# Kernel optimization log

Hardware: AMD Instinct MI355X
Metric: run time of the kernel (lower is better)

The kernel has to match this reference:

```python
import jax, jax.numpy as jnp
import numpy as np

D_IN, D_HID, N_TOK = 2048, 8192, 8192

def _ternary(key, shape):
    # ternary {-1, 0, 1} weights stored as float32
    return jax.random.randint(key, shape, -1, 2).astype(jnp.float32)

def setup_inputs() -> dict:
    key = jax.random.key(0)
    kx, k1, k2, kh, k3 = jax.random.split(key, 5)
    return {
        "x": jax.random.normal(kx, (N_TOK, D_IN), dtype=jnp.float32),
        "W1": _ternary(k1, (D_HID, D_IN)),   # gate proj
        "W2": _ternary(k2, (D_HID, D_IN)),   # value proj
        "Wh": _ternary(kh, (D_HID, D_HID)),  # hidden layer (depth-1 == 1)
        "W3": _ternary(k3, (D_IN, D_HID)),   # output proj
        # per-layer dequant scales (scalar), ~1/sqrt(fan_in)
        "s1": jnp.float32(1.0 / np.sqrt(D_IN)),
        "s2": jnp.float32(1.0 / np.sqrt(D_IN)),
        "sh": jnp.float32(1.0 / np.sqrt(D_HID)),
        "s3": jnp.float32(1.0 / np.sqrt(D_HID)),
    }

def _tlin(x, W, s):
    # ternary packed linear: dequantized matmul, no bias
    return jnp.einsum('td,hd->th', x, W) * s

def reference(x, W1, W2, Wh, W3, s1, s2, sh, s3):
    h = jax.nn.silu(_tlin(x, W1, s1)) * _tlin(x, W2, s2)   # SwiGLU entry
    h = jax.nn.gelu(_tlin(h, Wh, sh), approximate=False)    # hidden block (depth-1)
    return _tlin(h, W3, s3)                                 # [N_TOK, D_IN]
```

## Files before the change

### kernel.cpp

```cpp
#include <hip/hip_runtime.h>
#include <hip/hip_bf16.h>
#include <stdint.h>

typedef __bf16 bf16;
typedef __bf16 bf16x8 __attribute__((ext_vector_type(8)));
typedef float f32x4 __attribute__((ext_vector_type(4)));

typedef uint32_t __attribute__((address_space(1))) * gptr_as1;
typedef uint32_t __attribute__((address_space(3))) * lptr_as3;

__device__ __forceinline__ void async16(const void* g, void* l) {
    __builtin_amdgcn_global_load_lds((gptr_as1)(uintptr_t)g,
                                     (lptr_as3)(uintptr_t)l,
                                     16, 0, 0);
}

__device__ __forceinline__ void bar() {
    asm volatile("" ::: "memory");
    __builtin_amdgcn_s_barrier();
    asm volatile("" ::: "memory");
}

__global__ void cvt_f32_bf16_kernel(const float* __restrict__ src,
                                    bf16* __restrict__ dst, int n8) {
    int i = blockIdx.x * blockDim.x + threadIdx.x;
    if (i >= n8) return;
    const float4* s = reinterpret_cast<const float4*>(src);
    float4 a = s[2 * (size_t)i], b = s[2 * (size_t)i + 1];
    bf16x8 v;
    v[0] = (bf16)a.x; v[1] = (bf16)a.y; v[2] = (bf16)a.z; v[3] = (bf16)a.w;
    v[4] = (bf16)b.x; v[5] = (bf16)b.y; v[6] = (bf16)b.z; v[7] = (bf16)b.w;
    *reinterpret_cast<bf16x8*>(dst + (size_t)i * 8) = v;
}

__global__ __launch_bounds__(256, 2)
void gemm12_swiglu(const bf16* __restrict__ A, const bf16* __restrict__ B1,
                   const bf16* __restrict__ B2, bf16* __restrict__ H,
                   const float* __restrict__ s1p, const float* __restrict__ s2p,
                   int N, int K) {
    __shared__ __align__(16) bf16 As[128][64];
    __shared__ __align__(16) bf16 B1s[128][64];
    __shared__ __align__(16) bf16 B2s[128][64];

    const int tid = threadIdx.x;
    const int w = tid >> 6, l = tid & 63;
    const int bn = blockIdx.x, bm = blockIdx.y;
    const int wr = w >> 1, wc = w & 1;

    f32x4 acc1[4][4] = {};
    f32x4 acc2[4][4] = {};

    const int srow = w * 8 + (l >> 3);
    const int scol = (l & 7) * 8;
    const bf16* Ab  = A  + (size_t)(bm * 128 + srow) * K + scol;
    const bf16* B1b = B1 + (size_t)(bn * 128 + srow) * K + scol;
    const bf16* B2b = B2 + (size_t)(bn * 128 + srow) * K + scol;
    char* AsB  = (char*)&As[0][0]  + w * 1024;
    char* B1sB = (char*)&B1s[0][0] + w * 1024;
    char* B2sB = (char*)&B2s[0][0] + w * 1024;

    for (int k0 = 0; k0 < K; k0 += 64) {
#pragma unroll
        for (int r = 0; r < 4; ++r) {
            async16(Ab  + (size_t)r * 32 * K + k0, AsB  + r * 4096);
            async16(B1b + (size_t)r * 32 * K + k0, B1sB + r * 4096);
            async16(B2b + (size_t)r * 32 * K + k0, B2sB + r * 4096);
        }
        __syncthreads();
#pragma unroll
        for (int kk = 0; kk < 64; kk += 32) {
            const int kc = kk + (l >> 4) * 8;
            const int rr = l & 15;
            bf16x8 av[4], b1v[4], b2v[4];
#pragma unroll
            for (int i = 0; i < 4; ++i)
                av[i] = *reinterpret_cast<const bf16x8*>(&As[wr * 64 + i * 16 + rr][kc]);
#pragma unroll
            for (int j = 0; j < 4; ++j)
                b1v[j] = *reinterpret_cast<const bf16x8*>(&B1s[wc * 64 + j * 16 + rr][kc]);
#pragma unroll
            for (int j = 0; j < 4; ++j)
                b2v[j] = *reinterpret_cast<const bf16x8*>(&B2s[wc * 64 + j * 16 + rr][kc]);
#pragma unroll
            for (int i = 0; i < 4; ++i)
#pragma unroll
                for (int j = 0; j < 4; ++j) {
                    acc1[i][j] = __builtin_amdgcn_mfma_f32_16x16x32_bf16(av[i], b1v[j], acc1[i][j], 0, 0, 0);
                    acc2[i][j] = __builtin_amdgcn_mfma_f32_16x16x32_bf16(av[i], b2v[j], acc2[i][j], 0, 0, 0);
                }
        }
        __syncthreads();
    }

    const float s1 = s1p[0], s2 = s2p[0];
    const int row0 = bm * 128 + wr * 64 + (l >> 4) * 4;
    const int col0 = bn * 128 + wc * 64 + (l & 15);
#pragma unroll
    for (int i = 0; i < 4; ++i)
#pragma unroll
        for (int j = 0; j < 4; ++j)
#pragma unroll
            for (int q = 0; q < 4; ++q) {
                float g = acc1[i][j][q] * s1;
                float v = acc2[i][j][q] * s2;
                float sig = 1.0f / (1.0f + __expf(-g));
                H[(size_t)(row0 + i * 16 + q) * N + (col0 + j * 16)] = (bf16)(g * sig * v);
            }
}

template <int EPI>
__global__ __launch_bounds__(512, 1)
void gemm8p(const bf16* __restrict__ A, const bf16* __restrict__ B,
            void* __restrict__ Cout, const float* __restrict__ sp,
            int N, int K) {
    __shared__ __align__(16) char sm[131072];

    const int tid = threadIdx.x;
    const int w = tid >> 6, l = tid & 63;
    const int wr = w >> 2, wc = w & 3;

    const int gx = gridDim.x;
    const int nwg = gx * (int)gridDim.y;
    const int orig = blockIdx.y * gx + blockIdx.x;
    const int wg = (orig & 7) * (nwg >> 3) + (orig >> 3);
    const int bm = wg / gx, bn = wg % gx;

    const int NT = K >> 6;

    f32x4 acc[8][4] = {};

    char* const bufA0 = sm;
    char* const bufB0 = sm + 32768;
    char* const bufA1 = sm + 65536;
    char* const bufB1 = sm + 98304;
    const int arow = bm * 256, brow = bn * 256;

    const int srow_in = l >> 3;
    const int scolb = ((l & 7) ^ srow_in) << 4;
    auto STAGE = [&](char* ldsT, const bf16* g, int grow0, int kt, int r0) {
        const int rr = r0 + w * 8 + srow_in;
        const char* gp = (const char*)(g + (size_t)(grow0 + rr) * K + kt * 64) + scolb;
        async16(gp, ldsT + r0 * 128 + w * 1024);
    };

    const int rlane = l & 15;
    const int chi = (l >> 4) << 4;
    auto FRAG = [&](const char* tb, int row, int ks) -> bf16x8 {
        const int cb = (ks * 64 + chi) ^ ((row & 7) << 4);
        return *reinterpret_cast<const bf16x8*>(tb + row * 128 + cb);
    };

    STAGE(bufB0, B, brow, 0, 0);   STAGE(bufB0, B, brow, 0, 64);
    STAGE(bufB0, B, brow, 0, 128); STAGE(bufB0, B, brow, 0, 192);
    STAGE(bufA0, A, arow, 0, 0);   STAGE(bufA0, A, arow, 0, 128);
    STAGE(bufA0, A, arow, 0, 64);  STAGE(bufA0, A, arow, 0, 192);
    STAGE(bufB1, B, brow, 1, 0);   STAGE(bufB1, B, brow, 1, 64);
    STAGE(bufB1, B, brow, 1, 128); STAGE(bufB1, B, brow, 1, 192);
    STAGE(bufA1, A, arow, 1, 0);   STAGE(bufA1, A, arow, 1, 128);
    asm volatile("s_waitcnt vmcnt(6)" ::: "memory");
    bar();

    for (int kt = 0; kt < NT; ++kt) {
        char* cA = (kt & 1) ? bufA1 : bufA0;
        char* cB = (kt & 1) ? bufB1 : bufB0;
        char* nA = (kt & 1) ? bufA0 : bufA1;

        bf16x8 av[8], bv[8];
#pragma unroll
        for (int j = 0; j < 4; ++j)
#pragma unroll
            for (int ks = 0; ks < 2; ++ks)
                bv[j * 2 + ks] = FRAG(cB, wc * 64 + j * 16 + rlane, ks);
#pragma unroll
        for (int i = 0; i < 4; ++i)
#pragma unroll
            for (int ks = 0; ks < 2; ++ks)
                av[i * 2 + ks] = FRAG(cA, wr * 128 + i * 16 + rlane, ks);
        if (kt + 1 < NT) { STAGE(nA, A, arow, kt + 1, 64); STAGE(nA, A, arow, kt + 1, 192); }
        bar();
        asm volatile("s_waitcnt lgkmcnt(0)" ::: "memory");
        __builtin_amdgcn_sched_barrier(0);
        __builtin_amdgcn_s_setprio(1);
#pragma unroll
        for (int i = 0; i < 4; ++i)
#pragma unroll
            for (int j = 0; j < 2; ++j)
#pragma unroll
                for (int ks = 0; ks < 2; ++ks)
                    acc[i][j] = __builtin_amdgcn_mfma_f32_16x16x32_bf16(av[i * 2 + ks], bv[j * 2 + ks], acc[i][j], 0, 0, 0);
        __builtin_amdgcn_s_setprio(0);
        bar();
        if (kt + 2 < NT) { STAGE(cB, B, brow, kt + 2, 0); STAGE(cB, B, brow, kt + 2, 64); }
        bar();
        __builtin_amdgcn_s_setprio(1);
#pragma unroll
        for (int i = 0; i < 4; ++i)
#pragma unroll
            for (int j = 2; j < 4; ++j)
#pragma unroll
                for (int ks = 0; ks < 2; ++ks)
                    acc[i][j] = __builtin_amdgcn_mfma_f32_16x16x32_bf16(av[i * 2 + ks], bv[j * 2 + ks], acc[i][j], 0, 0, 0);
        __builtin_amdgcn_s_setprio(0);
        bar();
        bf16x8 ah[8];
#pragma unroll
        for (int i = 0; i < 4; ++i)
#pragma unroll
            for (int ks = 0; ks < 2; ++ks)
                ah[i * 2 + ks] = FRAG(cA, wr * 128 + 64 + i * 16 + rlane, ks);
        if (kt + 2 < NT) { STAGE(cB, B, brow, kt + 2, 128); STAGE(cB, B, brow, kt + 2, 192); }
        bar();
        asm volatile("s_waitcnt lgkmcnt(0)" ::: "memory");
        __builtin_amdgcn_sched_barrier(0);
        __builtin_amdgcn_s_setprio(1);
#pragma unroll
        for (int i = 0; i < 4; ++i)
#pragma unroll
            for (int j = 0; j < 2; ++j)
#pragma unroll
                for (int ks = 0; ks < 2; ++ks)
                    acc[4 + i][j] = __builtin_amdgcn_mfma_f32_16x16x32_bf16(ah[i * 2 + ks], bv[j * 2 + ks], acc[4 + i][j], 0, 0, 0);
        __builtin_amdgcn_s_setprio(0);
        bar();
        if (kt + 2 < NT) { STAGE(cA, A, arow, kt + 2, 0); STAGE(cA, A, arow, kt + 2, 128); }
        bar();
        __builtin_amdgcn_s_setprio(1);
#pragma unroll
        for (int i = 0; i < 4; ++i)
#pragma unroll
            for (int j = 2; j < 4; ++j)
#pragma unroll
                for (int ks = 0; ks < 2; ++ks)
                    acc[4 + i][j] = __builtin_amdgcn_mfma_f32_16x16x32_bf16(ah[i * 2 + ks], bv[j * 2 + ks], acc[4 + i][j], 0, 0, 0);
        __builtin_amdgcn_s_setprio(0);
        if (kt == NT - 2) { asm volatile("s_waitcnt vmcnt(0)" ::: "memory"); }
        else              { asm volatile("s_waitcnt vmcnt(6)" ::: "memory"); }
        bar();
    }

    const float s = sp[0];
    const int r0 = bm * 256 + wr * 128 + ((l >> 4) << 2);
    const int c0 = bn * 256 + wc * 64 + rlane;
#pragma unroll
    for (int i = 0; i < 8; ++i)
#pragma unroll
        for (int j = 0; j < 4; ++j)
#pragma unroll
            for (int q = 0; q < 4; ++q) {
                float v = acc[i][j][q] * s;
                size_t idx = (size_t)(r0 + i * 16 + q) * N + (c0 + j * 16);
                if constexpr (EPI == 0) {
                    float g = 0.5f * v * (1.0f + erff(v * 0.70710678118654752f));
                    ((bf16*)Cout)[idx] = (bf16)g;
                } else {
                    ((float*)Cout)[idx] = v;
                }
            }
}

extern "C" void kernel_launch(void* const* d_in, const int* in_sizes, int n_in,
                              void* d_out, int out_size, void* d_ws, size_t ws_size,
                              hipStream_t stream) {
    constexpr int NTOK = 8192, DIN = 2048, DHID = 8192;

    const float* x  = (const float*)d_in[0];
    const float* W1 = (const float*)d_in[1];
    const float* W2 = (const float*)d_in[2];
    const float* Wh = (const float*)d_in[3];
    const float* W3 = (const float*)d_in[4];
    const float* s1 = (const float*)d_in[5];
    const float* s2 = (const float*)d_in[6];
    const float* sh = (const float*)d_in[7];
    const float* s3 = (const float*)d_in[8];
    float* out = (float*)d_out;

    char* ws = (char*)d_ws;
    size_t off = 0;
    bf16* xb  = (bf16*)(ws + off); off += (size_t)NTOK * DIN * 2;
    bf16* w1b = (bf16*)(ws + off); off += (size_t)DHID * DIN * 2;
    bf16* w2b = (bf16*)(ws + off); off += (size_t)DHID * DIN * 2;
    bf16* w3b = (bf16*)(ws + off); off += (size_t)DIN * DHID * 2;
    bf16* whb = (bf16*)(ws + off); off += (size_t)DHID * DHID * 2;
    bf16* h1  = (bf16*)(ws + off); off += (size_t)NTOK * DHID * 2;
    bf16* h2  = (bf16*)(ws + off); off += (size_t)NTOK * DHID * 2;
    if (ws_size < off) return;

    auto cvt = [&](const float* s, bf16* d, size_t n) {
        int n8 = (int)(n / 8);
        cvt_f32_bf16_kernel<<<(n8 + 255) / 256, 256, 0, stream>>>(s, d, n8);
    };
    cvt(x,  xb,  (size_t)NTOK * DIN);
    cvt(W1, w1b, (size_t)DHID * DIN);
    cvt(W2, w2b, (size_t)DHID * DIN);
    cvt(W3, w3b, (size_t)DIN * DHID);
    cvt(Wh, whb, (size_t)DHID * DHID);

    gemm12_swiglu<<<dim3(DHID / 128, NTOK / 128), 256, 0, stream>>>(
        xb, w1b, w2b, h1, s1, s2, DHID, DIN);
    gemm8p<0><<<dim3(DHID / 256, NTOK / 256), 512, 0, stream>>>(
        h1, whb, h2, sh, DHID, DHID);
    gemm8p<1><<<dim3(DIN / 256, NTOK / 256), 512, 0, stream>>>(
        h2, w3b, out, s3, DIN, DHID);
}
```

Before: 1.886 ms.

## Fuse gate/value GEMM into pipelined kernel via interleaved W1/W2 layout

Drops the simple 128x128 SwiGLU GEMM kernel. W1 and W2 are now converted into one interleaved weight buffer, alternating 16-row blocks of gate and value rows, so the optimized 256x256 double-buffered gemm8p kernel can run the first layer with a SwiGLU epilogue that pairs adjacent accumulator tiles. The main loop is also reordered into quadrant-wise fragment loads with explicit buffer swapping, and K becomes a template constant. The aim is to replace the slower first-layer kernel with the better-pipelined one, at the cost of a more intricate staging and wait schedule.

```diff
diff --git a/kernel.cpp b/kernel.cpp
--- a/kernel.cpp
+++ b/kernel.cpp
@@ -33,86 +33,26 @@
     *reinterpret_cast<bf16x8*>(dst + (size_t)i * 8) = v;
 }
 
-__global__ __launch_bounds__(256, 2)
-void gemm12_swiglu(const bf16* __restrict__ A, const bf16* __restrict__ B1,
-                   const bf16* __restrict__ B2, bf16* __restrict__ H,
-                   const float* __restrict__ s1p, const float* __restrict__ s2p,
-                   int N, int K) {
-    __shared__ __align__(16) bf16 As[128][64];
-    __shared__ __align__(16) bf16 B1s[128][64];
-    __shared__ __align__(16) bf16 B2s[128][64];
-
-    const int tid = threadIdx.x;
-    const int w = tid >> 6, l = tid & 63;
-    const int bn = blockIdx.x, bm = blockIdx.y;
-    const int wr = w >> 1, wc = w & 1;
-
-    f32x4 acc1[4][4] = {};
-    f32x4 acc2[4][4] = {};
-
-    const int srow = w * 8 + (l >> 3);
-    const int scol = (l & 7) * 8;
-    const bf16* Ab  = A  + (size_t)(bm * 128 + srow) * K + scol;
-    const bf16* B1b = B1 + (size_t)(bn * 128 + srow) * K + scol;
-    const bf16* B2b = B2 + (size_t)(bn * 128 + srow) * K + scol;
-    char* AsB  = (char*)&As[0][0]  + w * 1024;
-    char* B1sB = (char*)&B1s[0][0] + w * 1024;
-    char* B2sB = (char*)&B2s[0][0] + w * 1024;
-
-    for (int k0 = 0; k0 < K; k0 += 64) {
-#pragma unroll
-        for (int r = 0; r < 4; ++r) {
-            async16(Ab  + (size_t)r * 32 * K + k0, AsB  + r * 4096);
-            async16(B1b + (size_t)r * 32 * K + k0, B1sB + r * 4096);
-            async16(B2b + (size_t)r * 32 * K + k0, B2sB + r * 4096);
-        }
-        __syncthreads();
-#pragma unroll
-        for (int kk = 0; kk < 64; kk += 32) {
-            const int kc = kk + (l >> 4) * 8;
-            const int rr = l & 15;
-            bf16x8 av[4], b1v[4], b2v[4];
-#pragma unroll
-            for (int i = 0; i < 4; ++i)
-                av[i] = *reinterpret_cast<const bf16x8*>(&As[wr * 64 + i * 16 + rr][kc]);
-#pragma unroll
-            for (int j = 0; j < 4; ++j)
-                b1v[j] = *reinterpret_cast<const bf16x8*>(&B1s[wc * 64 + j * 16 + rr][kc]);
-#pragma unroll
-            for (int j = 0; j < 4; ++j)
-                b2v[j] = *reinterpret_cast<const bf16x8*>(&B2s[wc * 64 + j * 16 + rr][kc]);
-#pragma unroll
-            for (int i = 0; i < 4; ++i)
-#pragma unroll
-                for (int j = 0; j < 4; ++j) {
-                    acc1[i][j] = __builtin_amdgcn_mfma_f32_16x16x32_bf16(av[i], b1v[j], acc1[i][j], 0, 0, 0);
-                    acc2[i][j] = __builtin_amdgcn_mfma_f32_16x16x32_bf16(av[i], b2v[j], acc2[i][j], 0, 0, 0);
-                }
-        }
-        __syncthreads();
-    }
-
-    const float s1 = s1p[0], s2 = s2p[0];
-    const int row0 = bm * 128 + wr * 64 + (l >> 4) * 4;
-    const int col0 = bn * 128 + wc * 64 + (l & 15);
-#pragma unroll
-    for (int i = 0; i < 4; ++i)
-#pragma unroll
-        for (int j = 0; j < 4; ++j)
-#pragma unroll
-            for (int q = 0; q < 4; ++q) {
-                float g = acc1[i][j][q] * s1;
-                float v = acc2[i][j][q] * s2;
-                float sig = 1.0f / (1.0f + __expf(-g));
-                H[(size_t)(row0 + i * 16 + q) * N + (col0 + j * 16)] = (bf16)(g * sig * v);
-            }
-}
-
-template <int EPI>
+__global__ void cvt_ilv_kernel(const float* __restrict__ src,
+                               bf16* __restrict__ dst, int n8, int sel) {
+    int i = blockIdx.x * blockDim.x + threadIdx.x;
+    if (i >= n8) return;
+    const int row = i >> 8;
+    const int c = i & 255;
+    const int drow = ((row >> 4) << 5) + (sel << 4) + (row & 15);
+    const float4* s = reinterpret_cast<const float4*>(src);
+    float4 a = s[2 * (size_t)i], b = s[2 * (size_t)i + 1];
+    bf16x8 v;
+    v[0] = (bf16)a.x; v[1] = (bf16)a.y; v[2] = (bf16)a.z; v[3] = (bf16)a.w;
+    v[4] = (bf16)b.x; v[5] = (bf16)b.y; v[6] = (bf16)b.z; v[7] = (bf16)b.w;
+    *reinterpret_cast<bf16x8*>(dst + ((size_t)drow * 256 + c) * 8) = v;
+}
+
+template <int EPI, int K>
 __global__ __launch_bounds__(512, 1)
 void gemm8p(const bf16* __restrict__ A, const bf16* __restrict__ B,
-            void* __restrict__ Cout, const float* __restrict__ sp,
-            int N, int K) {
+            void* __restrict__ Cout, const float* __restrict__ s1p,
+            const float* __restrict__ s2p, int N, int ldh) {
     __shared__ __align__(16) char sm[131072];
 
     const int tid = threadIdx.x;
@@ -125,7 +65,7 @@
     const int wg = (orig & 7) * (nwg >> 3) + (orig >> 3);
     const int bm = wg / gx, bn = wg % gx;
 
-    const int NT = K >> 6;
+    constexpr int NT = K / 64;
 
     f32x4 acc[8][4] = {};
 
@@ -154,29 +94,30 @@
     STAGE(bufB0, B, brow, 0, 128); STAGE(bufB0, B, brow, 0, 192);
     STAGE(bufA0, A, arow, 0, 0);   STAGE(bufA0, A, arow, 0, 128);
     STAGE(bufA0, A, arow, 0, 64);  STAGE(bufA0, A, arow, 0, 192);
+    STAGE(bufA1, A, arow, 1, 0);   STAGE(bufA1, A, arow, 1, 128);
     STAGE(bufB1, B, brow, 1, 0);   STAGE(bufB1, B, brow, 1, 64);
     STAGE(bufB1, B, brow, 1, 128); STAGE(bufB1, B, brow, 1, 192);
-    STAGE(bufA1, A, arow, 1, 0);   STAGE(bufA1, A, arow, 1, 128);
     asm volatile("s_waitcnt vmcnt(6)" ::: "memory");
     bar();
 
+    char* cA = bufA0; char* cB = bufB0;
+    char* nA = bufA1; char* nB = bufB1;
+
+#pragma unroll 1
     for (int kt = 0; kt < NT; ++kt) {
-        char* cA = (kt & 1) ? bufA1 : bufA0;
-        char* cB = (kt & 1) ? bufB1 : bufB0;
-        char* nA = (kt & 1) ? bufA0 : bufA1;
-
-        bf16x8 av[8], bv[8];
-#pragma unroll
-        for (int j = 0; j < 4; ++j)
-#pragma unroll
-            for (int ks = 0; ks < 2; ++ks)
-                bv[j * 2 + ks] = FRAG(cB, wc * 64 + j * 16 + rlane, ks);
-#pragma unroll
-        for (int i = 0; i < 4; ++i)
-#pragma unroll
-            for (int ks = 0; ks < 2; ++ks)
-                av[i * 2 + ks] = FRAG(cA, wr * 128 + i * 16 + rlane, ks);
+        bf16x8 avl[8], bvl[4], bvh[4], avh[8];
+#pragma unroll
+        for (int i = 0; i < 4; ++i)
+#pragma unroll
+            for (int ks = 0; ks < 2; ++ks)
+                avl[i * 2 + ks] = FRAG(cA, wr * 128 + i * 16 + rlane, ks);
+#pragma unroll
+        for (int j = 0; j < 2; ++j)
+#pragma unroll
+            for (int ks = 0; ks < 2; ++ks)
+                bvl[j * 2 + ks] = FRAG(cB, wc * 64 + j * 16 + rlane, ks);
         if (kt + 1 < NT) { STAGE(nA, A, arow, kt + 1, 64); STAGE(nA, A, arow, kt + 1, 192); }
+        asm volatile("s_waitcnt lgkmcnt(8)" ::: "memory");
         bar();
         asm volatile("s_waitcnt lgkmcnt(0)" ::: "memory");
         __builtin_amdgcn_sched_barrier(0);
@@ -187,28 +128,15 @@
             for (int j = 0; j < 2; ++j)
 #pragma unroll
                 for (int ks = 0; ks < 2; ++ks)
-                    acc[i][j] = __builtin_amdgcn_mfma_f32_16x16x32_bf16(av[i * 2 + ks], bv[j * 2 + ks], acc[i][j], 0, 0, 0);
-        __builtin_amdgcn_s_setprio(0);
-        bar();
-        if (kt + 2 < NT) { STAGE(cB, B, brow, kt + 2, 0); STAGE(cB, B, brow, kt + 2, 64); }
-        bar();
-        __builtin_amdgcn_s_setprio(1);
-#pragma unroll
-        for (int i = 0; i < 4; ++i)
-#pragma unroll
-            for (int j = 2; j < 4; ++j)
-#pragma unroll
-                for (int ks = 0; ks < 2; ++ks)
-                    acc[i][j] = __builtin_amdgcn_mfma_f32_16x16x32_bf16(av[i * 2 + ks], bv[j * 2 + ks], acc[i][j], 0, 0, 0);
-        __builtin_amdgcn_s_setprio(0);
-        bar();
-        bf16x8 ah[8];
-#pragma unroll
-        for (int i = 0; i < 4; ++i)
-#pragma unroll
-            for (int ks = 0; ks < 2; ++ks)
-                ah[i * 2 + ks] = FRAG(cA, wr * 128 + 64 + i * 16 + rlane, ks);
-        if (kt + 2 < NT) { STAGE(cB, B, brow, kt + 2, 128); STAGE(cB, B, brow, kt + 2, 192); }
+                    acc[i][j] = __builtin_amdgcn_mfma_f32_16x16x32_bf16(avl[i * 2 + ks], bvl[j * 2 + ks], acc[i][j], 0, 0, 0);
+        __builtin_amdgcn_s_setprio(0);
+        bar();
+#pragma unroll
+        for (int j = 0; j < 2; ++j)
+#pragma unroll
+            for (int ks = 0; ks < 2; ++ks)
+                bvh[j * 2 + ks] = FRAG(cB, wc * 64 + 32 + j * 16 + rlane, ks);
+        if (kt + 2 < NT) { STAGE(cA, A, arow, kt + 2, 0); STAGE(cA, A, arow, kt + 2, 128); }
         bar();
         asm volatile("s_waitcnt lgkmcnt(0)" ::: "memory");
         __builtin_amdgcn_sched_barrier(0);
@@ -219,43 +147,81 @@
             for (int j = 0; j < 2; ++j)
 #pragma unroll
                 for (int ks = 0; ks < 2; ++ks)
-                    acc[4 + i][j] = __builtin_amdgcn_mfma_f32_16x16x32_bf16(ah[i * 2 + ks], bv[j * 2 + ks], acc[4 + i][j], 0, 0, 0);
-        __builtin_amdgcn_s_setprio(0);
-        bar();
-        if (kt + 2 < NT) { STAGE(cA, A, arow, kt + 2, 0); STAGE(cA, A, arow, kt + 2, 128); }
-        bar();
-        __builtin_amdgcn_s_setprio(1);
-#pragma unroll
-        for (int i = 0; i < 4; ++i)
-#pragma unroll
-            for (int j = 2; j < 4; ++j)
-#pragma unroll
-                for (int ks = 0; ks < 2; ++ks)
-                    acc[4 + i][j] = __builtin_amdgcn_mfma_f32_16x16x32_bf16(ah[i * 2 + ks], bv[j * 2 + ks], acc[4 + i][j], 0, 0, 0);
+                    acc[i][2 + j] = __builtin_amdgcn_mfma_f32_16x16x32_bf16(avl[i * 2 + ks], bvh[j * 2 + ks], acc[i][2 + j], 0, 0, 0);
+        __builtin_amdgcn_s_setprio(0);
+        bar();
+#pragma unroll
+        for (int i = 0; i < 4; ++i)
+#pragma unroll
+            for (int ks = 0; ks < 2; ++ks)
+                avh[i * 2 + ks] = FRAG(cA, wr * 128 + 64 + i * 16 + rlane, ks);
+        if (kt + 2 < NT) { STAGE(cB, B, brow, kt + 2, 0); STAGE(cB, B, brow, kt + 2, 64); }
+        bar();
+        asm volatile("s_waitcnt lgkmcnt(0)" ::: "memory");
+        __builtin_amdgcn_sched_barrier(0);
+        __builtin_amdgcn_s_setprio(1);
+#pragma unroll
+        for (int i = 0; i < 4; ++i)
+#pragma unroll
+            for (int j = 0; j < 2; ++j)
+#pragma unroll
+                for (int ks = 0; ks < 2; ++ks)
+                    acc[4 + i][j] = __builtin_amdgcn_mfma_f32_16x16x32_bf16(avh[i * 2 + ks], bvl[j * 2 + ks], acc[4 + i][j], 0, 0, 0);
+        __builtin_amdgcn_s_setprio(0);
+        bar();
+        if (kt + 2 < NT) { STAGE(cB, B, brow, kt + 2, 128); STAGE(cB, B, brow, kt + 2, 192); }
+        bar();
+        __builtin_amdgcn_s_setprio(1);
+#pragma unroll
+        for (int i = 0; i < 4; ++i)
+#pragma unroll
+            for (int j = 0; j < 2; ++j)
+#pragma unroll
+                for (int ks = 0; ks < 2; ++ks)
+                    acc[4 + i][2 + j] = __builtin_amdgcn_mfma_f32_16x16x32_bf16(avh[i * 2 + ks], bvh[j * 2 + ks], acc[4 + i][2 + j], 0, 0, 0);
         __builtin_amdgcn_s_setprio(0);
         if (kt == NT - 2) { asm volatile("s_waitcnt vmcnt(0)" ::: "memory"); }
         else              { asm volatile("s_waitcnt vmcnt(6)" ::: "memory"); }
         bar();
+        char* t = cA; cA = nA; nA = t;
+        t = cB; cB = nB; nB = t;
     }
 
-    const float s = sp[0];
+    const float s1 = s1p[0];
     const int r0 = bm * 256 + wr * 128 + ((l >> 4) << 2);
-    const int c0 = bn * 256 + wc * 64 + rlane;
-#pragma unroll
-    for (int i = 0; i < 8; ++i)
-#pragma unroll
-        for (int j = 0; j < 4; ++j)
-#pragma unroll
-            for (int q = 0; q < 4; ++q) {
-                float v = acc[i][j][q] * s;
-                size_t idx = (size_t)(r0 + i * 16 + q) * N + (c0 + j * 16);
-                if constexpr (EPI == 0) {
-                    float g = 0.5f * v * (1.0f + erff(v * 0.70710678118654752f));
-                    ((bf16*)Cout)[idx] = (bf16)g;
-                } else {
-                    ((float*)Cout)[idx] = v;
+    if constexpr (EPI == 2) {
+        const float s2 = s2p[0];
+        const int hcb = (bn * 8 + wc * 2) * 16 + rlane;
+#pragma unroll
+        for (int i = 0; i < 8; ++i)
+#pragma unroll
+            for (int jp = 0; jp < 2; ++jp)
+#pragma unroll
+                for (int q = 0; q < 4; ++q) {
+                    float g = acc[i][2 * jp][q] * s1;
+                    float v = acc[i][2 * jp + 1][q] * s2;
+                    float sig = 1.0f / (1.0f + __expf(-g));
+                    ((bf16*)Cout)[(size_t)(r0 + i * 16 + q) * ldh + hcb + jp * 16] =
+                        (bf16)(g * sig * v);
                 }
-            }
+    } else {
+        const int c0 = bn * 256 + wc * 64 + rlane;
+#pragma unroll
+        for (int i = 0; i < 8; ++i)
+#pragma unroll
+            for (int j = 0; j < 4; ++j)
+#pragma unroll
+                for (int q = 0; q < 4; ++q) {
+                    float v = acc[i][j][q] * s1;
+                    size_t idx = (size_t)(r0 + i * 16 + q) * N + (c0 + j * 16);
+                    if constexpr (EPI == 0) {
+                        float g = 0.5f * v * (1.0f + erff(v * 0.70710678118654752f));
+                        ((bf16*)Cout)[idx] = (bf16)g;
+                    } else {
+                        ((float*)Cout)[idx] = v;
+                    }
+                }
+    }
 }
 
 extern "C" void kernel_launch(void* const* d_in, const int* in_sizes, int n_in,
@@ -276,13 +242,12 @@
 
     char* ws = (char*)d_ws;
     size_t off = 0;
-    bf16* xb  = (bf16*)(ws + off); off += (size_t)NTOK * DIN * 2;
-    bf16* w1b = (bf16*)(ws + off); off += (size_t)DHID * DIN * 2;
-    bf16* w2b = (bf16*)(ws + off); off += (size_t)DHID * DIN * 2;
-    bf16* w3b = (bf16*)(ws + off); off += (size_t)DIN * DHID * 2;
-    bf16* whb = (bf16*)(ws + off); off += (size_t)DHID * DHID * 2;
-    bf16* h1  = (bf16*)(ws + off); off += (size_t)NTOK * DHID * 2;
-    bf16* h2  = (bf16*)(ws + off); off += (size_t)NTOK * DHID * 2;
+    bf16* xb   = (bf16*)(ws + off); off += (size_t)NTOK * DIN * 2;
+    bf16* w12b = (bf16*)(ws + off); off += (size_t)2 * DHID * DIN * 2;
+    bf16* w3b  = (bf16*)(ws + off); off += (size_t)DIN * DHID * 2;
+    bf16* whb  = (bf16*)(ws + off); off += (size_t)DHID * DHID * 2;
+    bf16* h1   = (bf16*)(ws + off); off += (size_t)NTOK * DHID * 2;
+    bf16* h2   = (bf16*)(ws + off); off += (size_t)NTOK * DHID * 2;
     if (ws_size < off) return;
 
     auto cvt = [&](const float* s, bf16* d, size_t n) {
@@ -290,15 +255,18 @@
         cvt_f32_bf16_kernel<<<(n8 + 255) / 256, 256, 0, stream>>>(s, d, n8);
     };
     cvt(x,  xb,  (size_t)NTOK * DIN);
-    cvt(W1, w1b, (size_t)DHID * DIN);
-    cvt(W2, w2b, (size_t)DHID * DIN);
+    cvt(Wh, whb, (size_t)DHID * DHID);
     cvt(W3, w3b, (size_t)DIN * DHID);
-    cvt(Wh, whb, (size_t)DHID * DHID);
-
-    gemm12_swiglu<<<dim3(DHID / 128, NTOK / 128), 256, 0, stream>>>(
-        xb, w1b, w2b, h1, s1, s2, DHID, DIN);
-    gemm8p<0><<<dim3(DHID / 256, NTOK / 256), 512, 0, stream>>>(
-        h1, whb, h2, sh, DHID, DHID);
-    gemm8p<1><<<dim3(DIN / 256, NTOK / 256), 512, 0, stream>>>(
-        h2, w3b, out, s3, DIN, DHID);
-}
+    {
+        int n8 = (int)((size_t)DHID * DIN / 8);
+        cvt_ilv_kernel<<<(n8 + 255) / 256, 256, 0, stream>>>(W1, w12b, n8, 0);
+        cvt_ilv_kernel<<<(n8 + 255) / 256, 256, 0, stream>>>(W2, w12b, n8, 1);
+    }
+
+    gemm8p<2, DIN><<<dim3(2 * DHID / 256, NTOK / 256), 512, 0, stream>>>(
+        xb, w12b, h1, s1, s2, 2 * DHID, DHID);
+    gemm8p<0, DHID><<<dim3(DHID / 256, NTOK / 256), 512, 0, stream>>>(
+        h1, whb, h2, sh, sh, DHID, DHID);
+    gemm8p<1, DHID><<<dim3(DIN / 256, NTOK / 256), 512, 0, stream>>>(
+        h2, w3b, out, s3, s3, DIN, DIN);
+}
```

Result: faster. 1.763 ms (-6.5%).
